# Kernel optimization log

Hardware: AMD Instinct MI355X
Metric: run time of the kernel (lower is better)

The kernel has to match this reference:

```python
import math
import jax, jax.numpy as jnp
import numpy as np

B, LQ, LK = 4, 128, 512
EMBED_TIME, NUM_HEADS, INPUT_DIM, HIDDEN_DIM = 128, 8, 64, 256
EK = EMBED_TIME // NUM_HEADS  # per-head time-embedding dim


def setup_inputs() -> dict:
    key = jax.random.key(0)
    ks = jax.random.split(key, 10)
    query = jax.random.normal(ks[0], (B, LQ, EMBED_TIME), dtype=jnp.float32)
    k_in = jax.random.normal(ks[1], (B, LK, EMBED_TIME), dtype=jnp.float32)
    value = jax.random.normal(ks[2], (B, LK, INPUT_DIM), dtype=jnp.float32)
    mask = jax.random.randint(ks[3], (B, LK, INPUT_DIM), 0, 2, dtype=jnp.int32)
    s_t = 1.0 / math.sqrt(EMBED_TIME)
    s_o = 1.0 / math.sqrt(NUM_HEADS * INPUT_DIM)
    Wq = jax.random.normal(ks[4], (EMBED_TIME, EMBED_TIME), dtype=jnp.float32) * s_t
    bq = jnp.zeros((EMBED_TIME,), dtype=jnp.float32)
    Wk = jax.random.normal(ks[5], (EMBED_TIME, EMBED_TIME), dtype=jnp.float32) * s_t
    bk = jnp.zeros((EMBED_TIME,), dtype=jnp.float32)
    Wo = jax.random.normal(ks[6], (NUM_HEADS * INPUT_DIM, HIDDEN_DIM), dtype=jnp.float32) * s_o
    bo = jnp.zeros((HIDDEN_DIM,), dtype=jnp.float32)
    return {"query": query, "key": k_in, "value": value, "mask": mask,
            "Wq": Wq, "bq": bq, "Wk": Wk, "bk": bk, "Wo": Wo, "bo": bo}


def reference(query, key, value, mask, Wq, bq, Wk, bk, Wo, bo):
    b, lq, _ = query.shape
    lk = key.shape[1]
    d = value.shape[-1]
    # project and split heads: [B, L, embed_time] -> [B, H, L, ek]
    q = (query @ Wq + bq).reshape(b, lq, NUM_HEADS, EK).transpose(0, 2, 1, 3)
    k = (key @ Wk + bk).reshape(b, lk, NUM_HEADS, EK).transpose(0, 2, 1, 3)
    # raw scores [B, H, Lq, Lk]
    scores = jnp.einsum("bhqe,bhke->bhqk", q, k) / math.sqrt(EK)
    # broadcast over value feature dim D and apply per-(time, feature) mask:
    # scores[..., None] -> [B,H,Lq,Lk,1], mask -> [B,1,1,Lk,D]
    m = mask[:, None, None, :, :]  # int 0/1
    scores_bd = jnp.where(m == 0, jnp.float32(-10000.0),
                          scores[..., None])  # [B,H,Lq,Lk,D]
    attn = jax.nn.softmax(scores_bd, axis=-2)  # softmax over Lk per feature
    # weighted sum over Lk with value [B,1,1,Lk,D] -> context [B,H,Lq,D]
    context = jnp.sum(attn * value[:, None, None, :, :], axis=-2)
    # merge heads: [B, Lq, H*D] and output projection
    context = context.transpose(0, 2, 1, 3).reshape(b, lq, NUM_HEADS * d)
    return context @ Wo + bo
```

## Files before the change

kernel.cpp:

```cpp
#include <hip/hip_runtime.h>
#include <math.h>

#define NB 4
#define LQ 128
#define LK 512
#define ET 128
#define NH 8
#define EKD 16
#define DD 64
#define HD 256

#define QP_OFF 0
#define KP_OFF (NB*LQ*ET)
#define CTX_OFF (KP_OFF + NB*LK*ET)

__global__ __launch_bounds__(256) void proj_kernel(
    const float* __restrict__ query, const float* __restrict__ key,
    const float* __restrict__ Wq, const float* __restrict__ bq,
    const float* __restrict__ Wk, const float* __restrict__ bk,
    float* __restrict__ ws)
{
  __shared__ float Xs[16][128];
  const int blk = blockIdx.x;
  const int tid = threadIdx.x;
  const float* X; const float* W; const float* bias; float* outp; int rowbase;
  if (blk < 32) { X = query; W = Wq; bias = bq; outp = ws + QP_OFF; rowbase = blk * 16; }
  else          { X = key;   W = Wk; bias = bk; outp = ws + KP_OFF; rowbase = (blk - 32) * 16; }

  for (int idx = tid; idx < 16 * 32; idx += 256) {
    int r = idx >> 5, c4 = idx & 31;
    ((float4*)(&Xs[r][0]))[c4] = ((const float4*)(X + (size_t)(rowbase + r) * ET))[c4];
  }
  __syncthreads();

  const int r  = tid >> 4;
  const int c0 = (tid & 15) * 8;
  float acc[8] = {0.f,0.f,0.f,0.f,0.f,0.f,0.f,0.f};
  #pragma unroll 4
  for (int kk = 0; kk < ET; ++kk) {
    float x = Xs[r][kk];
    const float* wrow = W + (size_t)kk * ET + c0;
    float4 w0 = *(const float4*)(wrow);
    float4 w1 = *(const float4*)(wrow + 4);
    acc[0] = fmaf(x, w0.x, acc[0]);
    acc[1] = fmaf(x, w0.y, acc[1]);
    acc[2] = fmaf(x, w0.z, acc[2]);
    acc[3] = fmaf(x, w0.w, acc[3]);
    acc[4] = fmaf(x, w1.x, acc[4]);
    acc[5] = fmaf(x, w1.y, acc[5]);
    acc[6] = fmaf(x, w1.z, acc[6]);
    acc[7] = fmaf(x, w1.w, acc[7]);
  }
  float4 bb0 = *(const float4*)(bias + c0);
  float4 bb1 = *(const float4*)(bias + c0 + 4);
  float* orow = outp + (size_t)(rowbase + r) * ET + c0;
  float4 o0 = make_float4(acc[0]+bb0.x, acc[1]+bb0.y, acc[2]+bb0.z, acc[3]+bb0.w);
  float4 o1 = make_float4(acc[4]+bb1.x, acc[5]+bb1.y, acc[6]+bb1.z, acc[7]+bb1.w);
  *(float4*)(orow)     = o0;
  *(float4*)(orow + 4) = o1;
}

__global__ __launch_bounds__(256) void attn_kernel(
    const float* __restrict__ value, const int* __restrict__ mask,
    float* __restrict__ ws)
{
  __shared__ float Buf[10240];
  __shared__ float Qs[16][16];
  __shared__ float Es[16][520];

  const float* Qp = ws + QP_OFF;
  const float* Kp = ws + KP_OFF;
  float* ctx = ws + CTX_OFF;

  const int bx = blockIdx.x;
  const int b  = bx >> 6;
  const int h  = (bx >> 3) & 7;
  const int qt = bx & 7;
  const int tid = threadIdx.x;

  for (int idx = tid; idx < LK * 4; idx += 256) {
    int k = idx >> 2, j4 = idx & 3;
    float4 v4 = *(const float4*)(Kp + (size_t)(b * LK + k) * ET + h * EKD + j4 * 4);
    *(float4*)(&Buf[k * 20 + j4 * 4]) = v4;
  }
  if (tid < 64) {
    int r = tid >> 2, j4 = tid & 3;
    *(float4*)(&Qs[r][j4 * 4]) =
        *(const float4*)(Qp + (size_t)(b * LQ + qt * 16 + r) * ET + h * EKD + j4 * 4);
  }
  __syncthreads();

  {
    const int r = tid >> 4;
    const int i = tid & 15;
    float qreg[16];
    #pragma unroll
    for (int j = 0; j < 16; ++j) qreg[j] = Qs[r][j];

    float sv[32];
    float smax = -1e30f;
    #pragma unroll 4
    for (int kk = 0; kk < 32; ++kk) {
      int k = kk * 16 + i;
      const float* kp = &Buf[k * 20];
      float4 k0 = *(const float4*)(kp);
      float4 k1 = *(const float4*)(kp + 4);
      float4 k2 = *(const float4*)(kp + 8);
      float4 k3 = *(const float4*)(kp + 12);
      float dot = qreg[0] * k0.x;
      dot = fmaf(qreg[1],  k0.y, dot);
      dot = fmaf(qreg[2],  k0.z, dot);
      dot = fmaf(qreg[3],  k0.w, dot);
      dot = fmaf(qreg[4],  k1.x, dot);
      dot = fmaf(qreg[5],  k1.y, dot);
      dot = fmaf(qreg[6],  k1.z, dot);
      dot = fmaf(qreg[7],  k1.w, dot);
      dot = fmaf(qreg[8],  k2.x, dot);
      dot = fmaf(qreg[9],  k2.y, dot);
      dot = fmaf(qreg[10], k2.z, dot);
      dot = fmaf(qreg[11], k2.w, dot);
      dot = fmaf(qreg[12], k3.x, dot);
      dot = fmaf(qreg[13], k3.y, dot);
      dot = fmaf(qreg[14], k3.z, dot);
      dot = fmaf(qreg[15], k3.w, dot);
      float s = dot * 0.25f;
      sv[kk] = s;
      smax = fmaxf(smax, s);
    }
    #pragma unroll
    for (int off = 1; off < 16; off <<= 1)
      smax = fmaxf(smax, __shfl_xor(smax, off));
    #pragma unroll
    for (int kk = 0; kk < 32; ++kk)
      Es[r][kk * 16 + i] = __expf(sv[kk] - smax);
  }
  __syncthreads();

  {
    const int w = tid >> 6;
    const int d = tid & 63;
    float num[16], den[16];
    #pragma unroll
    for (int r = 0; r < 16; ++r) { num[r] = 0.f; den[r] = 0.f; }

    const int*   mcol = mask  + (size_t)b * LK * DD + d;
    const float* vcol = value + (size_t)b * LK * DD + d;
    const int kbase = w * 128;

    #pragma unroll 2
    for (int kb = 0; kb < 32; ++kb) {
      const int k = kbase + kb * 4;
      float m0 = (float)mcol[(size_t)(k + 0) * DD];
      float m1 = (float)mcol[(size_t)(k + 1) * DD];
      float m2 = (float)mcol[(size_t)(k + 2) * DD];
      float m3 = (float)mcol[(size_t)(k + 3) * DD];
      float v0 = vcol[(size_t)(k + 0) * DD];
      float v1 = vcol[(size_t)(k + 1) * DD];
      float v2 = vcol[(size_t)(k + 2) * DD];
      float v3 = vcol[(size_t)(k + 3) * DD];
      float mv0 = m0 * v0, mv1 = m1 * v1, mv2 = m2 * v2, mv3 = m3 * v3;
      #pragma unroll
      for (int r = 0; r < 16; ++r) {
        float4 e = *(const float4*)(&Es[r][k]);
        num[r] = fmaf(e.x, mv0, num[r]);
        num[r] = fmaf(e.y, mv1, num[r]);
        num[r] = fmaf(e.z, mv2, num[r]);
        num[r] = fmaf(e.w, mv3, num[r]);
        den[r] = fmaf(e.x, m0, den[r]);
        den[r] = fmaf(e.y, m1, den[r]);
        den[r] = fmaf(e.z, m2, den[r]);
        den[r] = fmaf(e.w, m3, den[r]);
      }
    }
    #pragma unroll
    for (int r = 0; r < 16; ++r) {
      Buf[(w * 16 + r) * 64 + d]        = num[r];
      Buf[4096 + (w * 16 + r) * 64 + d] = den[r];
    }
  }
  __syncthreads();

  {
    const int d  = tid & 63;
    const int rg = tid >> 6;
    #pragma unroll
    for (int j = 0; j < 4; ++j) {
      const int r = rg * 4 + j;
      float n = Buf[(r)      * 64 + d] + Buf[(16 + r) * 64 + d]
              + Buf[(32 + r) * 64 + d] + Buf[(48 + r) * 64 + d];
      float dn = Buf[4096 + (r)      * 64 + d] + Buf[4096 + (16 + r) * 64 + d]
               + Buf[4096 + (32 + r) * 64 + d] + Buf[4096 + (48 + r) * 64 + d];
      const int row = b * LQ + qt * 16 + r;
      ctx[(size_t)row * (NH * DD) + h * DD + d] = n / dn;
    }
  }
}

__global__ __launch_bounds__(256) void outproj_kernel(
    const float* __restrict__ Wo, const float* __restrict__ bo,
    const float* __restrict__ ws, float* __restrict__ out)
{
  __shared__ float Cs[16][512];
  __shared__ float Pn[4][16][64];
  const float* ctx = ws + CTX_OFF;
  const int bx = blockIdx.x;
  const int rt = bx >> 2;
  const int ct = bx & 3;
  const int r0 = rt * 16, c0 = ct * 64;
  const int tid = threadIdx.x;

  for (int idx = tid; idx < 16 * 128; idx += 256) {
    int r = idx >> 7, c4 = idx & 127;
    *(float4*)(&Cs[r][c4 * 4]) = *(const float4*)(ctx + (size_t)(r0 + r) * 512 + c4 * 4);
  }
  __syncthreads();

  const int w    = tid >> 6;
  const int lane = tid & 63;
  const int c    = c0 + lane;
  float acc[16];
  #pragma unroll
  for (int r = 0; r < 16; ++r) acc[r] = 0.f;

  const int kbase = w * 128;
  #pragma unroll 2
  for (int kb = 0; kb < 32; ++kb) {
    const int k = kbase + kb * 4;
    float w0 = Wo[(size_t)(k + 0) * HD + c];
    float w1 = Wo[(size_t)(k + 1) * HD + c];
    float w2 = Wo[(size_t)(k + 2) * HD + c];
    float w3 = Wo[(size_t)(k + 3) * HD + c];
    #pragma unroll
    for (int r = 0; r < 16; ++r) {
      float4 cs = *(const float4*)(&Cs[r][k]);
      acc[r] = fmaf(cs.x, w0, acc[r]);
      acc[r] = fmaf(cs.y, w1, acc[r]);
      acc[r] = fmaf(cs.z, w2, acc[r]);
      acc[r] = fmaf(cs.w, w3, acc[r]);
    }
  }
  #pragma unroll
  for (int r = 0; r < 16; ++r) Pn[w][r][lane] = acc[r];
  __syncthreads();

  {
    const int rg = tid >> 6;
    const float bb = bo[c0 + (tid & 63)];
    #pragma unroll
    for (int j = 0; j < 4; ++j) {
      const int r = rg * 4 + j;
      float s = Pn[0][r][tid & 63] + Pn[1][r][tid & 63]
              + Pn[2][r][tid & 63] + Pn[3][r][tid & 63];
      out[(size_t)(r0 + r) * HD + c0 + (tid & 63)] = s + bb;
    }
  }
}

extern "C" void kernel_launch(void* const* d_in, const int* in_sizes, int n_in,
                              void* d_out, int out_size, void* d_ws, size_t ws_size,
                              hipStream_t stream) {
  const float* query = (const float*)d_in[0];
  const float* key   = (const float*)d_in[1];
  const float* value = (const float*)d_in[2];
  const int*   mask  = (const int*)d_in[3];
  const float* Wq    = (const float*)d_in[4];
  const float* bq    = (const float*)d_in[5];
  const float* Wk    = (const float*)d_in[6];
  const float* bk    = (const float*)d_in[7];
  const float* Wo    = (const float*)d_in[8];
  const float* bo    = (const float*)d_in[9];
  float* out = (float*)d_out;
  float* ws  = (float*)d_ws;

  proj_kernel<<<160, 256, 0, stream>>>(query, key, Wq, bq, Wk, bk, ws);
  attn_kernel<<<256, 256, 0, stream>>>(value, mask, ws);
  outproj_kernel<<<128, 256, 0, stream>>>(Wo, bo, ws, out);
}
```

Baseline: 125.0 us.

## Fuse three kernels into one cooperative kernel with grid-wide syncs

Replaces the three launches (projection, attention, output projection) with a single cooperative kernel of 256 blocks that separates the stages with grid.sync() and reuses one shared-memory buffer. The aim is to remove two kernel launch gaps and their inter-kernel drain. The cost is grid-barrier overhead, a larger shared-memory footprint for every block, and idle blocks in the first and last stages. Unroll factors and shared-memory padding are also adjusted.

```diff
diff --git a/kernel.cpp b/kernel.cpp
--- a/kernel.cpp
+++ b/kernel.cpp
@@ -1,5 +1,8 @@
 #include <hip/hip_runtime.h>
+#include <hip/hip_cooperative_groups.h>
 #include <math.h>
+
+namespace cg = cooperative_groups;
 
 #define NB 4
 #define LQ 128
@@ -14,244 +17,242 @@
 #define KP_OFF (NB*LQ*ET)
 #define CTX_OFF (KP_OFF + NB*LK*ET)
 
-__global__ __launch_bounds__(256) void proj_kernel(
+#define QS_B 10240
+#define ES_B 10496
+#define PN_B 8256
+
+__global__ __launch_bounds__(256) void fused_mta_kernel(
     const float* __restrict__ query, const float* __restrict__ key,
+    const float* __restrict__ value, const int* __restrict__ mask,
     const float* __restrict__ Wq, const float* __restrict__ bq,
     const float* __restrict__ Wk, const float* __restrict__ bk,
-    float* __restrict__ ws)
+    const float* __restrict__ Wo, const float* __restrict__ bo,
+    float* __restrict__ ws, float* __restrict__ out)
 {
-  __shared__ float Xs[16][128];
-  const int blk = blockIdx.x;
+  __shared__ __align__(16) float S[19200];
+  cg::grid_group grid = cg::this_grid();
+  const int bx  = blockIdx.x;
   const int tid = threadIdx.x;
-  const float* X; const float* W; const float* bias; float* outp; int rowbase;
-  if (blk < 32) { X = query; W = Wq; bias = bq; outp = ws + QP_OFF; rowbase = blk * 16; }
-  else          { X = key;   W = Wk; bias = bk; outp = ws + KP_OFF; rowbase = (blk - 32) * 16; }
-
-  for (int idx = tid; idx < 16 * 32; idx += 256) {
-    int r = idx >> 5, c4 = idx & 31;
-    ((float4*)(&Xs[r][0]))[c4] = ((const float4*)(X + (size_t)(rowbase + r) * ET))[c4];
+
+  if (bx < 160) {
+    const float* X; const float* W; const float* bias; float* outp; int rowbase;
+    if (bx < 32) { X = query; W = Wq; bias = bq; outp = ws + QP_OFF; rowbase = bx * 16; }
+    else         { X = key;   W = Wk; bias = bk; outp = ws + KP_OFF; rowbase = (bx - 32) * 16; }
+
+    for (int idx = tid; idx < 16 * 32; idx += 256) {
+      int r = idx >> 5, c4 = idx & 31;
+      *(float4*)(&S[r * 132 + c4 * 4]) =
+          ((const float4*)(X + (size_t)(rowbase + r) * ET))[c4];
+    }
+    __syncthreads();
+
+    const int r  = tid >> 4;
+    const int c0 = (tid & 15) * 8;
+    float acc[8] = {0.f,0.f,0.f,0.f,0.f,0.f,0.f,0.f};
+    #pragma unroll 8
+    for (int kk = 0; kk < ET; ++kk) {
+      float x = S[r * 132 + kk];
+      const float* wrow = W + (size_t)kk * ET + c0;
+      float4 w0 = *(const float4*)(wrow);
+      float4 w1 = *(const float4*)(wrow + 4);
+      acc[0] = fmaf(x, w0.x, acc[0]);
+      acc[1] = fmaf(x, w0.y, acc[1]);
+      acc[2] = fmaf(x, w0.z, acc[2]);
+      acc[3] = fmaf(x, w0.w, acc[3]);
+      acc[4] = fmaf(x, w1.x, acc[4]);
+      acc[5] = fmaf(x, w1.y, acc[5]);
+      acc[6] = fmaf(x, w1.z, acc[6]);
+      acc[7] = fmaf(x, w1.w, acc[7]);
+    }
+    float4 bb0 = *(const float4*)(bias + c0);
+    float4 bb1 = *(const float4*)(bias + c0 + 4);
+    float* orow = outp + (size_t)(rowbase + r) * ET + c0;
+    *(float4*)(orow)     = make_float4(acc[0]+bb0.x, acc[1]+bb0.y, acc[2]+bb0.z, acc[3]+bb0.w);
+    *(float4*)(orow + 4) = make_float4(acc[4]+bb1.x, acc[5]+bb1.y, acc[6]+bb1.z, acc[7]+bb1.w);
   }
-  __syncthreads();
-
-  const int r  = tid >> 4;
-  const int c0 = (tid & 15) * 8;
-  float acc[8] = {0.f,0.f,0.f,0.f,0.f,0.f,0.f,0.f};
-  #pragma unroll 4
-  for (int kk = 0; kk < ET; ++kk) {
-    float x = Xs[r][kk];
-    const float* wrow = W + (size_t)kk * ET + c0;
-    float4 w0 = *(const float4*)(wrow);
-    float4 w1 = *(const float4*)(wrow + 4);
-    acc[0] = fmaf(x, w0.x, acc[0]);
-    acc[1] = fmaf(x, w0.y, acc[1]);
-    acc[2] = fmaf(x, w0.z, acc[2]);
-    acc[3] = fmaf(x, w0.w, acc[3]);
-    acc[4] = fmaf(x, w1.x, acc[4]);
-    acc[5] = fmaf(x, w1.y, acc[5]);
-    acc[6] = fmaf(x, w1.z, acc[6]);
-    acc[7] = fmaf(x, w1.w, acc[7]);
+  grid.sync();
+
+  {
+    const float* Qp = ws + QP_OFF;
+    const float* Kp = ws + KP_OFF;
+    float* ctx = ws + CTX_OFF;
+
+    const int b  = bx >> 6;
+    const int h  = (bx >> 3) & 7;
+    const int qt = bx & 7;
+
+    for (int idx = tid; idx < LK * 4; idx += 256) {
+      int k = idx >> 2, j4 = idx & 3;
+      float4 v4 = *(const float4*)(Kp + (size_t)(b * LK + k) * ET + h * EKD + j4 * 4);
+      *(float4*)(&S[k * 20 + j4 * 4]) = v4;
+    }
+    if (tid < 64) {
+      int r = tid >> 2, j4 = tid & 3;
+      *(float4*)(&S[QS_B + r * 16 + j4 * 4]) =
+          *(const float4*)(Qp + (size_t)(b * LQ + qt * 16 + r) * ET + h * EKD + j4 * 4);
+    }
+    __syncthreads();
+
+    {
+      const int r = tid >> 4;
+      const int i = tid & 15;
+      float qreg[16];
+      #pragma unroll
+      for (int j = 0; j < 16; ++j) qreg[j] = S[QS_B + r * 16 + j];
+
+      float sv[32];
+      float smax = -1e30f;
+      #pragma unroll 4
+      for (int kk = 0; kk < 32; ++kk) {
+        int k = kk * 16 + i;
+        const float* kp = &S[k * 20];
+        float4 k0 = *(const float4*)(kp);
+        float4 k1 = *(const float4*)(kp + 4);
+        float4 k2 = *(const float4*)(kp + 8);
+        float4 k3 = *(const float4*)(kp + 12);
+        float dot = qreg[0] * k0.x;
+        dot = fmaf(qreg[1],  k0.y, dot);
+        dot = fmaf(qreg[2],  k0.z, dot);
+        dot = fmaf(qreg[3],  k0.w, dot);
+        dot = fmaf(qreg[4],  k1.x, dot);
+        dot = fmaf(qreg[5],  k1.y, dot);
+        dot = fmaf(qreg[6],  k1.z, dot);
+        dot = fmaf(qreg[7],  k1.w, dot);
+        dot = fmaf(qreg[8],  k2.x, dot);
+        dot = fmaf(qreg[9],  k2.y, dot);
+        dot = fmaf(qreg[10], k2.z, dot);
+        dot = fmaf(qreg[11], k2.w, dot);
+        dot = fmaf(qreg[12], k3.x, dot);
+        dot = fmaf(qreg[13], k3.y, dot);
+        dot = fmaf(qreg[14], k3.z, dot);
+        dot = fmaf(qreg[15], k3.w, dot);
+        float s = dot * 0.25f;
+        sv[kk] = s;
+        smax = fmaxf(smax, s);
+      }
+      #pragma unroll
+      for (int off = 1; off < 16; off <<= 1)
+        smax = fmaxf(smax, __shfl_xor(smax, off));
+      #pragma unroll
+      for (int kk = 0; kk < 32; ++kk)
+        S[ES_B + r * 520 + kk * 16 + i] = __expf(sv[kk] - smax);
+    }
+    __syncthreads();
+
+    {
+      const int w = tid >> 6;
+      const int d = tid & 63;
+      float num[16], den[16];
+      #pragma unroll
+      for (int r = 0; r < 16; ++r) { num[r] = 0.f; den[r] = 0.f; }
+
+      const int*   mcol = mask  + (size_t)b * LK * DD + d;
+      const float* vcol = value + (size_t)b * LK * DD + d;
+      const int kbase = w * 128;
+
+      #pragma unroll 2
+      for (int kb = 0; kb < 32; ++kb) {
+        const int k = kbase + kb * 4;
+        float m0 = (float)mcol[(size_t)(k + 0) * DD];
+        float m1 = (float)mcol[(size_t)(k + 1) * DD];
+        float m2 = (float)mcol[(size_t)(k + 2) * DD];
+        float m3 = (float)mcol[(size_t)(k + 3) * DD];
+        float v0 = vcol[(size_t)(k + 0) * DD];
+        float v1 = vcol[(size_t)(k + 1) * DD];
+        float v2 = vcol[(size_t)(k + 2) * DD];
+        float v3 = vcol[(size_t)(k + 3) * DD];
+        float mv0 = m0 * v0, mv1 = m1 * v1, mv2 = m2 * v2, mv3 = m3 * v3;
+        #pragma unroll
+        for (int r = 0; r < 16; ++r) {
+          float4 e = *(const float4*)(&S[ES_B + r * 520 + k]);
+          num[r] = fmaf(e.x, mv0, num[r]);
+          num[r] = fmaf(e.y, mv1, num[r]);
+          num[r] = fmaf(e.z, mv2, num[r]);
+          num[r] = fmaf(e.w, mv3, num[r]);
+          den[r] = fmaf(e.x, m0, den[r]);
+          den[r] = fmaf(e.y, m1, den[r]);
+          den[r] = fmaf(e.z, m2, den[r]);
+          den[r] = fmaf(e.w, m3, den[r]);
+        }
+      }
+      #pragma unroll
+      for (int r = 0; r < 16; ++r) {
+        S[(w * 16 + r) * 64 + d]        = num[r];
+        S[4096 + (w * 16 + r) * 64 + d] = den[r];
+      }
+    }
+    __syncthreads();
+
+    {
+      const int d  = tid & 63;
+      const int rg = tid >> 6;
+      #pragma unroll
+      for (int j = 0; j < 4; ++j) {
+        const int r = rg * 4 + j;
+        float n  = S[(r)      * 64 + d] + S[(16 + r) * 64 + d]
+                 + S[(32 + r) * 64 + d] + S[(48 + r) * 64 + d];
+        float dn = S[4096 + (r)      * 64 + d] + S[4096 + (16 + r) * 64 + d]
+                 + S[4096 + (32 + r) * 64 + d] + S[4096 + (48 + r) * 64 + d];
+        const int row = b * LQ + qt * 16 + r;
+        ctx[(size_t)row * (NH * DD) + h * DD + d] = n / dn;
+      }
+    }
   }
-  float4 bb0 = *(const float4*)(bias + c0);
-  float4 bb1 = *(const float4*)(bias + c0 + 4);
-  float* orow = outp + (size_t)(rowbase + r) * ET + c0;
-  float4 o0 = make_float4(acc[0]+bb0.x, acc[1]+bb0.y, acc[2]+bb0.z, acc[3]+bb0.w);
-  float4 o1 = make_float4(acc[4]+bb1.x, acc[5]+bb1.y, acc[6]+bb1.z, acc[7]+bb1.w);
-  *(float4*)(orow)     = o0;
-  *(float4*)(orow + 4) = o1;
-}
-
-__global__ __launch_bounds__(256) void attn_kernel(
-    const float* __restrict__ value, const int* __restrict__ mask,
-    float* __restrict__ ws)
-{
-  __shared__ float Buf[10240];
-  __shared__ float Qs[16][16];
-  __shared__ float Es[16][520];
-
-  const float* Qp = ws + QP_OFF;
-  const float* Kp = ws + KP_OFF;
-  float* ctx = ws + CTX_OFF;
-
-  const int bx = blockIdx.x;
-  const int b  = bx >> 6;
-  const int h  = (bx >> 3) & 7;
-  const int qt = bx & 7;
-  const int tid = threadIdx.x;
-
-  for (int idx = tid; idx < LK * 4; idx += 256) {
-    int k = idx >> 2, j4 = idx & 3;
-    float4 v4 = *(const float4*)(Kp + (size_t)(b * LK + k) * ET + h * EKD + j4 * 4);
-    *(float4*)(&Buf[k * 20 + j4 * 4]) = v4;
-  }
-  if (tid < 64) {
-    int r = tid >> 2, j4 = tid & 3;
-    *(float4*)(&Qs[r][j4 * 4]) =
-        *(const float4*)(Qp + (size_t)(b * LQ + qt * 16 + r) * ET + h * EKD + j4 * 4);
-  }
-  __syncthreads();
-
-  {
-    const int r = tid >> 4;
-    const int i = tid & 15;
-    float qreg[16];
+  grid.sync();
+
+  if (bx < 128) {
+    const float* ctx = ws + CTX_OFF;
+    const int rt = bx >> 2;
+    const int ct = bx & 3;
+    const int r0 = rt * 16, c0 = ct * 64;
+
+    for (int idx = tid; idx < 16 * 128; idx += 256) {
+      int r = idx >> 7, c4 = idx & 127;
+      *(float4*)(&S[r * 516 + c4 * 4]) =
+          *(const float4*)(ctx + (size_t)(r0 + r) * 512 + c4 * 4);
+    }
+    __syncthreads();
+
+    const int w    = tid >> 6;
+    const int lane = tid & 63;
+    const int c    = c0 + lane;
+    float acc[16];
     #pragma unroll
-    for (int j = 0; j < 16; ++j) qreg[j] = Qs[r][j];
-
-    float sv[32];
-    float smax = -1e30f;
+    for (int r = 0; r < 16; ++r) acc[r] = 0.f;
+
+    const int kbase = w * 128;
     #pragma unroll 4
-    for (int kk = 0; kk < 32; ++kk) {
-      int k = kk * 16 + i;
-      const float* kp = &Buf[k * 20];
-      float4 k0 = *(const float4*)(kp);
-      float4 k1 = *(const float4*)(kp + 4);
-      float4 k2 = *(const float4*)(kp + 8);
-      float4 k3 = *(const float4*)(kp + 12);
-      float dot = qreg[0] * k0.x;
-      dot = fmaf(qreg[1],  k0.y, dot);
-      dot = fmaf(qreg[2],  k0.z, dot);
-      dot = fmaf(qreg[3],  k0.w, dot);
-      dot = fmaf(qreg[4],  k1.x, dot);
-      dot = fmaf(qreg[5],  k1.y, dot);
-      dot = fmaf(qreg[6],  k1.z, dot);
-      dot = fmaf(qreg[7],  k1.w, dot);
-      dot = fmaf(qreg[8],  k2.x, dot);
-      dot = fmaf(qreg[9],  k2.y, dot);
-      dot = fmaf(qreg[10], k2.z, dot);
-      dot = fmaf(qreg[11], k2.w, dot);
-      dot = fmaf(qreg[12], k3.x, dot);
-      dot = fmaf(qreg[13], k3.y, dot);
-      dot = fmaf(qreg[14], k3.z, dot);
-      dot = fmaf(qreg[15], k3.w, dot);
-      float s = dot * 0.25f;
-      sv[kk] = s;
-      smax = fmaxf(smax, s);
-    }
-    #pragma unroll
-    for (int off = 1; off < 16; off <<= 1)
-      smax = fmaxf(smax, __shfl_xor(smax, off));
-    #pragma unroll
-    for (int kk = 0; kk < 32; ++kk)
-      Es[r][kk * 16 + i] = __expf(sv[kk] - smax);
-  }
-  __syncthreads();
-
-  {
-    const int w = tid >> 6;
-    const int d = tid & 63;
-    float num[16], den[16];
-    #pragma unroll
-    for (int r = 0; r < 16; ++r) { num[r] = 0.f; den[r] = 0.f; }
-
-    const int*   mcol = mask  + (size_t)b * LK * DD + d;
-    const float* vcol = value + (size_t)b * LK * DD + d;
-    const int kbase = w * 128;
-
-    #pragma unroll 2
     for (int kb = 0; kb < 32; ++kb) {
       const int k = kbase + kb * 4;
-      float m0 = (float)mcol[(size_t)(k + 0) * DD];
-      float m1 = (float)mcol[(size_t)(k + 1) * DD];
-      float m2 = (float)mcol[(size_t)(k + 2) * DD];
-      float m3 = (float)mcol[(size_t)(k + 3) * DD];
-      float v0 = vcol[(size_t)(k + 0) * DD];
-      float v1 = vcol[(size_t)(k + 1) * DD];
-      float v2 = vcol[(size_t)(k + 2) * DD];
-      float v3 = vcol[(size_t)(k + 3) * DD];
-      float mv0 = m0 * v0, mv1 = m1 * v1, mv2 = m2 * v2, mv3 = m3 * v3;
+      float w0 = Wo[(size_t)(k + 0) * HD + c];
+      float w1 = Wo[(size_t)(k + 1) * HD + c];
+      float w2 = Wo[(size_t)(k + 2) * HD + c];
+      float w3 = Wo[(size_t)(k + 3) * HD + c];
       #pragma unroll
       for (int r = 0; r < 16; ++r) {
-        float4 e = *(const float4*)(&Es[r][k]);
-        num[r] = fmaf(e.x, mv0, num[r]);
-        num[r] = fmaf(e.y, mv1, num[r]);
-        num[r] = fmaf(e.z, mv2, num[r]);
-        num[r] = fmaf(e.w, mv3, num[r]);
-        den[r] = fmaf(e.x, m0, den[r]);
-        den[r] = fmaf(e.y, m1, den[r]);
-        den[r] = fmaf(e.z, m2, den[r]);
-        den[r] = fmaf(e.w, m3, den[r]);
+        float4 cs = *(const float4*)(&S[r * 516 + k]);
+        acc[r] = fmaf(cs.x, w0, acc[r]);
+        acc[r] = fmaf(cs.y, w1, acc[r]);
+        acc[r] = fmaf(cs.z, w2, acc[r]);
+        acc[r] = fmaf(cs.w, w3, acc[r]);
       }
     }
     #pragma unroll
-    for (int r = 0; r < 16; ++r) {
-      Buf[(w * 16 + r) * 64 + d]        = num[r];
-      Buf[4096 + (w * 16 + r) * 64 + d] = den[r];
-    }
-  }
-  __syncthreads();
-
-  {
-    const int d  = tid & 63;
-    const int rg = tid >> 6;
-    #pragma unroll
-    for (int j = 0; j < 4; ++j) {
-      const int r = rg * 4 + j;
-      float n = Buf[(r)      * 64 + d] + Buf[(16 + r) * 64 + d]
-              + Buf[(32 + r) * 64 + d] + Buf[(48 + r) * 64 + d];
-      float dn = Buf[4096 + (r)      * 64 + d] + Buf[4096 + (16 + r) * 64 + d]
-               + Buf[4096 + (32 + r) * 64 + d] + Buf[4096 + (48 + r) * 64 + d];
-      const int row = b * LQ + qt * 16 + r;
-      ctx[(size_t)row * (NH * DD) + h * DD + d] = n / dn;
-    }
-  }
-}
-
-__global__ __launch_bounds__(256) void outproj_kernel(
-    const float* __restrict__ Wo, const float* __restrict__ bo,
-    const float* __restrict__ ws, float* __restrict__ out)
-{
-  __shared__ float Cs[16][512];
-  __shared__ float Pn[4][16][64];
-  const float* ctx = ws + CTX_OFF;
-  const int bx = blockIdx.x;
-  const int rt = bx >> 2;
-  const int ct = bx & 3;
-  const int r0 = rt * 16, c0 = ct * 64;
-  const int tid = threadIdx.x;
-
-  for (int idx = tid; idx < 16 * 128; idx += 256) {
-    int r = idx >> 7, c4 = idx & 127;
-    *(float4*)(&Cs[r][c4 * 4]) = *(const float4*)(ctx + (size_t)(r0 + r) * 512 + c4 * 4);
-  }
-  __syncthreads();
-
-  const int w    = tid >> 6;
-  const int lane = tid & 63;
-  const int c    = c0 + lane;
-  float acc[16];
-  #pragma unroll
-  for (int r = 0; r < 16; ++r) acc[r] = 0.f;
-
-  const int kbase = w * 128;
-  #pragma unroll 2
-  for (int kb = 0; kb < 32; ++kb) {
-    const int k = kbase + kb * 4;
-    float w0 = Wo[(size_t)(k + 0) * HD + c];
-    float w1 = Wo[(size_t)(k + 1) * HD + c];
-    float w2 = Wo[(size_t)(k + 2) * HD + c];
-    float w3 = Wo[(size_t)(k + 3) * HD + c];
-    #pragma unroll
-    for (int r = 0; r < 16; ++r) {
-      float4 cs = *(const float4*)(&Cs[r][k]);
-      acc[r] = fmaf(cs.x, w0, acc[r]);
-      acc[r] = fmaf(cs.y, w1, acc[r]);
-      acc[r] = fmaf(cs.z, w2, acc[r]);
-      acc[r] = fmaf(cs.w, w3, acc[r]);
-    }
-  }
-  #pragma unroll
-  for (int r = 0; r < 16; ++r) Pn[w][r][lane] = acc[r];
-  __syncthreads();
-
-  {
-    const int rg = tid >> 6;
-    const float bb = bo[c0 + (tid & 63)];
-    #pragma unroll
-    for (int j = 0; j < 4; ++j) {
-      const int r = rg * 4 + j;
-      float s = Pn[0][r][tid & 63] + Pn[1][r][tid & 63]
-              + Pn[2][r][tid & 63] + Pn[3][r][tid & 63];
-      out[(size_t)(r0 + r) * HD + c0 + (tid & 63)] = s + bb;
+    for (int r = 0; r < 16; ++r) S[PN_B + (w * 16 + r) * 64 + lane] = acc[r];
+    __syncthreads();
+
+    {
+      const int rg = tid >> 6;
+      const float bb = bo[c0 + (tid & 63)];
+      #pragma unroll
+      for (int j = 0; j < 4; ++j) {
+        const int r = rg * 4 + j;
+        float s = S[PN_B + (r)      * 64 + (tid & 63)]
+                + S[PN_B + (16 + r) * 64 + (tid & 63)]
+                + S[PN_B + (32 + r) * 64 + (tid & 63)]
+                + S[PN_B + (48 + r) * 64 + (tid & 63)];
+        out[(size_t)(r0 + r) * HD + c0 + (tid & 63)] = s + bb;
+      }
     }
   }
 }
@@ -272,7 +273,11 @@
   float* out = (float*)d_out;
   float* ws  = (float*)d_ws;
 
-  proj_kernel<<<160, 256, 0, stream>>>(query, key, Wq, bq, Wk, bk, ws);
-  attn_kernel<<<256, 256, 0, stream>>>(value, mask, ws);
-  outproj_kernel<<<128, 256, 0, stream>>>(Wo, bo, ws, out);
+  void* kargs[] = {
+    (void*)&query, (void*)&key, (void*)&value, (void*)&mask,
+    (void*)&Wq, (void*)&bq, (void*)&Wk, (void*)&bk,
+    (void*)&Wo, (void*)&bo, (void*)&ws, (void*)&out
+  };
+  hipLaunchCooperativeKernel((void*)fused_mta_kernel,
+                             dim3(256), dim3(256), kargs, 0, stream);
 }
```

Result: slower. 232.4 us (+85.9%).

## Halve attention and out-projection tiles to double grid size; head-major K layout

Applied to the files above, without the earlier changes.

The attention kernel now processes 8 query rows per block instead of 16, doubling the grid to 512 blocks, and the output projection uses 32-column tiles, doubling its grid to 256 blocks. Both aim to fill more of the GPU's compute units. The key projection writes K in a per-(batch, head) contiguous layout so each attention block loads its K slice with contiguous float4 reads. Smaller tiles mean mask and value (and Wo) are re-read from global memory twice as often in total, and some unroll factors and shared-memory padding are also adjusted.

```diff
diff --git a/kernel.cpp b/kernel.cpp
--- a/kernel.cpp
+++ b/kernel.cpp
@@ -11,8 +11,11 @@
 #define HD 256
 
 #define QP_OFF 0
-#define KP_OFF (NB*LQ*ET)
-#define CTX_OFF (KP_OFF + NB*LK*ET)
+#define KPB_OFF (NB*LQ*ET)
+#define CTX_OFF (KPB_OFF + NB*NH*LK*EKD)
+
+#define QS_B 10240
+#define ES_B 10496
 
 __global__ __launch_bounds__(256) void proj_kernel(
     const float* __restrict__ query, const float* __restrict__ key,
@@ -20,23 +23,24 @@
     const float* __restrict__ Wk, const float* __restrict__ bk,
     float* __restrict__ ws)
 {
-  __shared__ float Xs[16][128];
+  __shared__ float Xs[16][132];
   const int blk = blockIdx.x;
   const int tid = threadIdx.x;
-  const float* X; const float* W; const float* bias; float* outp; int rowbase;
-  if (blk < 32) { X = query; W = Wq; bias = bq; outp = ws + QP_OFF; rowbase = blk * 16; }
-  else          { X = key;   W = Wk; bias = bk; outp = ws + KP_OFF; rowbase = (blk - 32) * 16; }
+  const bool isQ = (blk < 32);
+  const float* X; const float* W; const float* bias; int rowbase;
+  if (isQ) { X = query; W = Wq; bias = bq; rowbase = blk * 16; }
+  else     { X = key;   W = Wk; bias = bk; rowbase = (blk - 32) * 16; }
 
   for (int idx = tid; idx < 16 * 32; idx += 256) {
     int r = idx >> 5, c4 = idx & 31;
-    ((float4*)(&Xs[r][0]))[c4] = ((const float4*)(X + (size_t)(rowbase + r) * ET))[c4];
+    *(float4*)(&Xs[r][c4 * 4]) = ((const float4*)(X + (size_t)(rowbase + r) * ET))[c4];
   }
   __syncthreads();
 
   const int r  = tid >> 4;
   const int c0 = (tid & 15) * 8;
   float acc[8] = {0.f,0.f,0.f,0.f,0.f,0.f,0.f,0.f};
-  #pragma unroll 4
+  #pragma unroll 8
   for (int kk = 0; kk < ET; ++kk) {
     float x = Xs[r][kk];
     const float* wrow = W + (size_t)kk * ET + c0;
@@ -53,56 +57,65 @@
   }
   float4 bb0 = *(const float4*)(bias + c0);
   float4 bb1 = *(const float4*)(bias + c0 + 4);
-  float* orow = outp + (size_t)(rowbase + r) * ET + c0;
   float4 o0 = make_float4(acc[0]+bb0.x, acc[1]+bb0.y, acc[2]+bb0.z, acc[3]+bb0.w);
   float4 o1 = make_float4(acc[4]+bb1.x, acc[5]+bb1.y, acc[6]+bb1.z, acc[7]+bb1.w);
-  *(float4*)(orow)     = o0;
-  *(float4*)(orow + 4) = o1;
+
+  if (isQ) {
+    float* orow = ws + QP_OFF + (size_t)(rowbase + r) * ET + c0;
+    *(float4*)(orow)     = o0;
+    *(float4*)(orow + 4) = o1;
+  } else {
+    const int row  = rowbase + r;
+    const int b    = row >> 9;
+    const int krow = row & 511;
+    const int h    = c0 >> 4;
+    const int cin  = c0 & 15;
+    float* dst = ws + KPB_OFF + ((size_t)(b * NH + h) * LK + krow) * EKD + cin;
+    *(float4*)(dst)     = o0;
+    *(float4*)(dst + 4) = o1;
+  }
 }
 
 __global__ __launch_bounds__(256) void attn_kernel(
     const float* __restrict__ value, const int* __restrict__ mask,
     float* __restrict__ ws)
 {
-  __shared__ float Buf[10240];
-  __shared__ float Qs[16][16];
-  __shared__ float Es[16][520];
+  __shared__ __align__(16) float S[14656];
+  const int bx  = blockIdx.x;
+  const int tid = threadIdx.x;
+  const int b  = bx >> 7;
+  const int h  = (bx >> 4) & 7;
+  const int qt = bx & 15;
 
   const float* Qp = ws + QP_OFF;
-  const float* Kp = ws + KP_OFF;
+  const float* Kb = ws + KPB_OFF + (size_t)(b * NH + h) * LK * EKD;
   float* ctx = ws + CTX_OFF;
 
-  const int bx = blockIdx.x;
-  const int b  = bx >> 6;
-  const int h  = (bx >> 3) & 7;
-  const int qt = bx & 7;
-  const int tid = threadIdx.x;
-
-  for (int idx = tid; idx < LK * 4; idx += 256) {
+  for (int idx = tid; idx < 2048; idx += 256) {
     int k = idx >> 2, j4 = idx & 3;
-    float4 v4 = *(const float4*)(Kp + (size_t)(b * LK + k) * ET + h * EKD + j4 * 4);
-    *(float4*)(&Buf[k * 20 + j4 * 4]) = v4;
-  }
-  if (tid < 64) {
+    float4 v4 = *(const float4*)(Kb + (size_t)idx * 4);
+    *(float4*)(&S[k * 20 + j4 * 4]) = v4;
+  }
+  if (tid < 32) {
     int r = tid >> 2, j4 = tid & 3;
-    *(float4*)(&Qs[r][j4 * 4]) =
-        *(const float4*)(Qp + (size_t)(b * LQ + qt * 16 + r) * ET + h * EKD + j4 * 4);
-  }
-  __syncthreads();
-
-  {
-    const int r = tid >> 4;
-    const int i = tid & 15;
+    *(float4*)(&S[QS_B + r * 16 + j4 * 4]) =
+        *(const float4*)(Qp + (size_t)(b * LQ + qt * 8 + r) * ET + h * EKD + j4 * 4);
+  }
+  __syncthreads();
+
+  {
+    const int r = tid >> 5;
+    const int i = tid & 31;
     float qreg[16];
     #pragma unroll
-    for (int j = 0; j < 16; ++j) qreg[j] = Qs[r][j];
-
-    float sv[32];
+    for (int j = 0; j < 16; ++j) qreg[j] = S[QS_B + r * 16 + j];
+
+    float sv[16];
     float smax = -1e30f;
     #pragma unroll 4
-    for (int kk = 0; kk < 32; ++kk) {
-      int k = kk * 16 + i;
-      const float* kp = &Buf[k * 20];
+    for (int kk = 0; kk < 16; ++kk) {
+      int k = kk * 32 + i;
+      const float* kp = &S[k * 20];
       float4 k0 = *(const float4*)(kp);
       float4 k1 = *(const float4*)(kp + 4);
       float4 k2 = *(const float4*)(kp + 8);
@@ -128,26 +141,26 @@
       smax = fmaxf(smax, s);
     }
     #pragma unroll
-    for (int off = 1; off < 16; off <<= 1)
+    for (int off = 1; off < 32; off <<= 1)
       smax = fmaxf(smax, __shfl_xor(smax, off));
     #pragma unroll
-    for (int kk = 0; kk < 32; ++kk)
-      Es[r][kk * 16 + i] = __expf(sv[kk] - smax);
+    for (int kk = 0; kk < 16; ++kk)
+      S[ES_B + r * 520 + kk * 32 + i] = __expf(sv[kk] - smax);
   }
   __syncthreads();
 
   {
     const int w = tid >> 6;
     const int d = tid & 63;
-    float num[16], den[16];
-    #pragma unroll
-    for (int r = 0; r < 16; ++r) { num[r] = 0.f; den[r] = 0.f; }
+    float num[8], den[8];
+    #pragma unroll
+    for (int r = 0; r < 8; ++r) { num[r] = 0.f; den[r] = 0.f; }
 
     const int*   mcol = mask  + (size_t)b * LK * DD + d;
     const float* vcol = value + (size_t)b * LK * DD + d;
     const int kbase = w * 128;
 
-    #pragma unroll 2
+    #pragma unroll 4
     for (int kb = 0; kb < 32; ++kb) {
       const int k = kbase + kb * 4;
       float m0 = (float)mcol[(size_t)(k + 0) * DD];
@@ -160,8 +173,8 @@
       float v3 = vcol[(size_t)(k + 3) * DD];
       float mv0 = m0 * v0, mv1 = m1 * v1, mv2 = m2 * v2, mv3 = m3 * v3;
       #pragma unroll
-      for (int r = 0; r < 16; ++r) {
-        float4 e = *(const float4*)(&Es[r][k]);
+      for (int r = 0; r < 8; ++r) {
+        float4 e = *(const float4*)(&S[ES_B + r * 520 + k]);
         num[r] = fmaf(e.x, mv0, num[r]);
         num[r] = fmaf(e.y, mv1, num[r]);
         num[r] = fmaf(e.z, mv2, num[r]);
@@ -173,9 +186,9 @@
       }
     }
     #pragma unroll
-    for (int r = 0; r < 16; ++r) {
-      Buf[(w * 16 + r) * 64 + d]        = num[r];
-      Buf[4096 + (w * 16 + r) * 64 + d] = den[r];
+    for (int r = 0; r < 8; ++r) {
+      S[(w * 8 + r) * 64 + d]        = num[r];
+      S[2048 + (w * 8 + r) * 64 + d] = den[r];
     }
   }
   __syncthreads();
@@ -184,13 +197,13 @@
     const int d  = tid & 63;
     const int rg = tid >> 6;
     #pragma unroll
-    for (int j = 0; j < 4; ++j) {
-      const int r = rg * 4 + j;
-      float n = Buf[(r)      * 64 + d] + Buf[(16 + r) * 64 + d]
-              + Buf[(32 + r) * 64 + d] + Buf[(48 + r) * 64 + d];
-      float dn = Buf[4096 + (r)      * 64 + d] + Buf[4096 + (16 + r) * 64 + d]
-               + Buf[4096 + (32 + r) * 64 + d] + Buf[4096 + (48 + r) * 64 + d];
-      const int row = b * LQ + qt * 16 + r;
+    for (int j = 0; j < 2; ++j) {
+      const int r = rg * 2 + j;
+      float n  = S[(r) * 64 + d]        + S[(8 + r) * 64 + d]
+               + S[(16 + r) * 64 + d]   + S[(24 + r) * 64 + d];
+      float dn = S[2048 + (r) * 64 + d] + S[2048 + (8 + r) * 64 + d]
+               + S[2048 + (16 + r) * 64 + d] + S[2048 + (24 + r) * 64 + d];
+      const int row = b * LQ + qt * 8 + r;
       ctx[(size_t)row * (NH * DD) + h * DD + d] = n / dn;
     }
   }
@@ -200,30 +213,32 @@
     const float* __restrict__ Wo, const float* __restrict__ bo,
     const float* __restrict__ ws, float* __restrict__ out)
 {
-  __shared__ float Cs[16][512];
-  __shared__ float Pn[4][16][64];
+  __shared__ __align__(16) float S[10304];
   const float* ctx = ws + CTX_OFF;
   const int bx = blockIdx.x;
-  const int rt = bx >> 2;
-  const int ct = bx & 3;
-  const int r0 = rt * 16, c0 = ct * 64;
+  const int rt = bx >> 3;
+  const int ct = bx & 7;
+  const int r0 = rt * 16, c0 = ct * 32;
   const int tid = threadIdx.x;
 
   for (int idx = tid; idx < 16 * 128; idx += 256) {
     int r = idx >> 7, c4 = idx & 127;
-    *(float4*)(&Cs[r][c4 * 4]) = *(const float4*)(ctx + (size_t)(r0 + r) * 512 + c4 * 4);
+    *(float4*)(&S[r * 516 + c4 * 4]) =
+        *(const float4*)(ctx + (size_t)(r0 + r) * 512 + c4 * 4);
   }
   __syncthreads();
 
   const int w    = tid >> 6;
   const int lane = tid & 63;
-  const int c    = c0 + lane;
-  float acc[16];
+  const int rh   = lane >> 5;
+  const int cc   = lane & 31;
+  const int c    = c0 + cc;
+  float acc[8];
   #pragma unroll
-  for (int r = 0; r < 16; ++r) acc[r] = 0.f;
+  for (int r = 0; r < 8; ++r) acc[r] = 0.f;
 
   const int kbase = w * 128;
-  #pragma unroll 2
+  #pragma unroll 4
   for (int kb = 0; kb < 32; ++kb) {
     const int k = kbase + kb * 4;
     float w0 = Wo[(size_t)(k + 0) * HD + c];
@@ -231,8 +246,9 @@
     float w2 = Wo[(size_t)(k + 2) * HD + c];
     float w3 = Wo[(size_t)(k + 3) * HD + c];
     #pragma unroll
-    for (int r = 0; r < 16; ++r) {
-      float4 cs = *(const float4*)(&Cs[r][k]);
+    for (int r = 0; r < 8; ++r) {
+      const int row = rh * 8 + r;
+      float4 cs = *(const float4*)(&S[row * 516 + k]);
       acc[r] = fmaf(cs.x, w0, acc[r]);
       acc[r] = fmaf(cs.y, w1, acc[r]);
       acc[r] = fmaf(cs.z, w2, acc[r]);
@@ -240,18 +256,21 @@
     }
   }
   #pragma unroll
-  for (int r = 0; r < 16; ++r) Pn[w][r][lane] = acc[r];
-  __syncthreads();
-
-  {
-    const int rg = tid >> 6;
-    const float bb = bo[c0 + (tid & 63)];
-    #pragma unroll
-    for (int j = 0; j < 4; ++j) {
-      const int r = rg * 4 + j;
-      float s = Pn[0][r][tid & 63] + Pn[1][r][tid & 63]
-              + Pn[2][r][tid & 63] + Pn[3][r][tid & 63];
-      out[(size_t)(r0 + r) * HD + c0 + (tid & 63)] = s + bb;
+  for (int r = 0; r < 8; ++r)
+    S[8256 + ((size_t)w * 16 + rh * 8 + r) * 32 + cc] = acc[r];
+  __syncthreads();
+
+  {
+    const int row = tid >> 4;
+    const int cc0 = (tid & 15) * 2;
+    #pragma unroll
+    for (int j = 0; j < 2; ++j) {
+      const int ccj = cc0 + j;
+      float s = S[8256 + (0 * 16 + row) * 32 + ccj]
+              + S[8256 + (1 * 16 + row) * 32 + ccj]
+              + S[8256 + (2 * 16 + row) * 32 + ccj]
+              + S[8256 + (3 * 16 + row) * 32 + ccj];
+      out[(size_t)(r0 + row) * HD + c0 + ccj] = s + bo[c0 + ccj];
     }
   }
 }
@@ -273,6 +292,6 @@
   float* ws  = (float*)d_ws;
 
   proj_kernel<<<160, 256, 0, stream>>>(query, key, Wq, bq, Wk, bk, ws);
-  attn_kernel<<<256, 256, 0, stream>>>(value, mask, ws);
-  outproj_kernel<<<128, 256, 0, stream>>>(Wo, bo, ws, out);
-}
+  attn_kernel<<<512, 256, 0, stream>>>(value, mask, ws);
+  outproj_kernel<<<256, 256, 0, stream>>>(Wo, bo, ws, out);
+}
```

New measurement: 114.0 us. -8.8%, faster.
